# Optimization experiments

Measured on AMD Instinct MI355X. Metric: run time of the kernel, lower is better.

The kernel has to match this reference:

```python
import jax, jax.numpy as jnp
import numpy as np

B, N, D, C = 32, 6, 41, 64
FH, FW = 4, 6            # 150//32, 200//32
IN_CH = 768
NX, NY, NZ = 200, 200, 1 # from x/y/zbound
DX = np.array([0.5, 0.5, 20.0], np.float32)
BX = np.array([-49.75, -49.75, 0.0], np.float32)  # bound[0] + step/2


def _frustum():
    # (D, FH, FW, 3) pixel-coord + depth frustum, matching create_frustum
    ds = np.arange(4.0, 45.0, 1.0, dtype=np.float32)             # D = 41
    xs = np.linspace(0.0, 200.0 - 1.0, FW, dtype=np.float32)
    ys = np.linspace(0.0, 150.0 - 1.0, FH, dtype=np.float32)
    g = np.stack(np.broadcast_arrays(xs[None, None, :], ys[None, :, None], ds[:, None, None]), axis=-1)
    return jnp.asarray(g)


def setup_inputs() -> dict:
    key = jax.random.key(0)
    k1, k2, k3 = jax.random.split(key, 3)
    x = jax.random.normal(k1, (B, N, IN_CH, FH, FW), jnp.float32)
    # cam-to-ego base rotation (cam z -> ego x, cam x -> -ego y, cam y -> -ego z)
    R0 = np.array([[0., 0., 1.], [-1., 0., 0.], [0., -1., 0.]], np.float32)
    yaw = 2.0 * np.pi * np.arange(N) / N
    cz, sz = np.cos(yaw).astype(np.float32), np.sin(yaw).astype(np.float32)
    Rz = np.zeros((N, 3, 3), np.float32)
    Rz[:, 0, 0] = cz; Rz[:, 0, 1] = -sz; Rz[:, 1, 0] = sz; Rz[:, 1, 1] = cz; Rz[:, 2, 2] = 1.0
    rots = jnp.asarray(np.broadcast_to((Rz @ R0)[None], (B, N, 3, 3)))
    K = np.array([[100., 0., 100.], [0., 100., 75.], [0., 0., 1.]], np.float32)
    intrins = jnp.asarray(np.broadcast_to(K, (B, N, 3, 3)))
    trans = jax.random.uniform(k2, (B, N, 3), jnp.float32, -2.0, 2.0)
    conv_w = jax.random.normal(k3, (D + C, IN_CH), jnp.float32) * 0.02
    conv_b = jnp.zeros((D + C,), jnp.float32)
    return {"x": x, "rots": rots, "trans": trans, "intrins": intrins, "conv_w": conv_w, "conv_b": conv_b}


def reference(x, rots, trans, intrins, conv_w, conv_b):
    frustum = _frustum()                                        # (D,FH,FW,3)
    # --- get_geometry ---
    pts = jnp.concatenate([frustum[..., :2] * frustum[..., 2:3], frustum[..., 2:3]], -1)
    combine = rots @ jnp.linalg.inv(intrins)                    # (B,N,3,3)
    geom = jnp.einsum('bnij,dhwj->bndhwi', combine, pts) + trans[:, :, None, None, None, :]
    # --- get_cam_feats: 1x1 conv depthnet, softmax depth, outer product ---
    xf = x.reshape(B * N, IN_CH, FH, FW)
    y = jnp.einsum('oc,bchw->bohw', conv_w, xf) + conv_b[None, :, None, None]
    depth_logit = y[:, :D]                                      # (BN,D,FH,FW)
    depth = jax.nn.softmax(depth_logit, axis=1)
    feat = y[:, D:D + C]                                        # (BN,C,FH,FW)
    xv = (depth[:, None] * feat[:, :, None]).reshape(B, N, C, D, FH, FW).transpose(0, 1, 3, 4, 5, 2)
    # --- voxel_pooling: segment-sum over voxel rank, scatter to BEV ---
    xN = xv.reshape(-1, C)                                      # (Nprime, C)
    g = ((geom - (BX - DX / 2.0)) / DX).astype(jnp.int32).reshape(-1, 3)  # trunc like .long()
    Np = xN.shape[0]
    bix = jnp.repeat(jnp.arange(Np // (Np // B) * 0 + B), Np // B)        # batch index per point
    kept = ((g[:, 0] >= 0) & (g[:, 0] < NX) & (g[:, 1] >= 0) & (g[:, 1] < NY)
            & (g[:, 2] >= 0) & (g[:, 2] < NZ))
    idx = ((bix * NZ + g[:, 2]) * NX + g[:, 0]) * NY + g[:, 1]
    idx = jnp.where(kept, idx, 0)
    xm = jnp.where(kept[:, None], xN, 0.0)
    pooled = jax.ops.segment_sum(xm, idx, num_segments=B * NZ * NX * NY)  # (B*NZ*NX*NY, C)
    final = pooled.reshape(B, NZ, NX, NY, C).transpose(0, 1, 4, 2, 3).reshape(B, NZ * C, NX, NY)
    return (final, depth_logit)
```

## Files before the change

### kernel.cpp

```cpp
#include <hip/hip_runtime.h>
#include <hip/hip_bf16.h>

#define B_    32
#define N_    6
#define D_    41
#define C_    64
#define FH_   4
#define FW_   6
#define INCH  768
#define HW    24
#define O_    105
#define PBN   984
#define PPB   5904
#define NPTS  188928
#define FINAL_ELEMS 81920000
#define NSEG  8
#define SEGV  5000
#define CONVB 192


__global__ __launch_bounds__(256) void k_fused(
    const float* __restrict__ x, const float* __restrict__ w,
    const float* __restrict__ bias,
    const float* __restrict__ m1, const float* __restrict__ trans,
    const float* __restrict__ m2,
    float* __restrict__ feat_ws, float* __restrict__ depth_ws,
    float* __restrict__ dlogit,
    int* __restrict__ cnt, unsigned* __restrict__ entries)
{
    __shared__ float xs[9216];
    __shared__ float ys[O_ * HW];
    __shared__ float smax[HW], srs[HW];

    const int t = threadIdx.x;

    if (blockIdx.x < CONVB) {
        const int bn = blockIdx.x;
        const int og = t / 6;
        const int q6 = t % 6;

        float a[3][4] = {{0.f,0.f,0.f,0.f},{0.f,0.f,0.f,0.f},{0.f,0.f,0.f,0.f}};
        const int o0 = og * 3;
        const float4* wr0 = (const float4*)(w + (size_t)(o0 + 0) * INCH);
        const float4* wr1 = (const float4*)(w + (size_t)(o0 + 1) * INCH);
        const float4* wr2 = (const float4*)(w + (size_t)(o0 + 2) * INCH);
        float4* xs4 = (float4*)xs;

        for (int half = 0; half < 2; ++half) {
            if (half) __syncthreads();
            const float4* xg = (const float4*)(x + (size_t)bn * (INCH * HW)) + half * 2304;
            for (int i = t; i < 2304; i += 256) xs4[i] = xg[i];
            __syncthreads();

            if (t < 210) {
                const int wb = half * 96;
                for (int c4 = 0; c4 < 96; ++c4) {
                    float4 w0 = wr0[wb + c4];
                    float4 w1 = wr1[wb + c4];
                    float4 w2 = wr2[wb + c4];
                    int cb = c4 * 4;
                    float4 x0 = xs4[(cb + 0) * 6 + q6];
                    float4 x1 = xs4[(cb + 1) * 6 + q6];
                    float4 x2 = xs4[(cb + 2) * 6 + q6];
                    float4 x3 = xs4[(cb + 3) * 6 + q6];
                    a[0][0]=fmaf(w0.x,x0.x,a[0][0]); a[0][1]=fmaf(w0.x,x0.y,a[0][1]);
                    a[0][2]=fmaf(w0.x,x0.z,a[0][2]); a[0][3]=fmaf(w0.x,x0.w,a[0][3]);
                    a[1][0]=fmaf(w1.x,x0.x,a[1][0]); a[1][1]=fmaf(w1.x,x0.y,a[1][1]);
                    a[1][2]=fmaf(w1.x,x0.z,a[1][2]); a[1][3]=fmaf(w1.x,x0.w,a[1][3]);
                    a[2][0]=fmaf(w2.x,x0.x,a[2][0]); a[2][1]=fmaf(w2.x,x0.y,a[2][1]);
                    a[2][2]=fmaf(w2.x,x0.z,a[2][2]); a[2][3]=fmaf(w2.x,x0.w,a[2][3]);
                    a[0][0]=fmaf(w0.y,x1.x,a[0][0]); a[0][1]=fmaf(w0.y,x1.y,a[0][1]);
                    a[0][2]=fmaf(w0.y,x1.z,a[0][2]); a[0][3]=fmaf(w0.y,x1.w,a[0][3]);
                    a[1][0]=fmaf(w1.y,x1.x,a[1][0]); a[1][1]=fmaf(w1.y,x1.y,a[1][1]);
                    a[1][2]=fmaf(w1.y,x1.z,a[1][2]); a[1][3]=fmaf(w1.y,x1.w,a[1][3]);
                    a[2][0]=fmaf(w2.y,x1.x,a[2][0]); a[2][1]=fmaf(w2.y,x1.y,a[2][1]);
                    a[2][2]=fmaf(w2.y,x1.z,a[2][2]); a[2][3]=fmaf(w2.y,x1.w,a[2][3]);
                    a[0][0]=fmaf(w0.z,x2.x,a[0][0]); a[0][1]=fmaf(w0.z,x2.y,a[0][1]);
                    a[0][2]=fmaf(w0.z,x2.z,a[0][2]); a[0][3]=fmaf(w0.z,x2.w,a[0][3]);
                    a[1][0]=fmaf(w1.z,x2.x,a[1][0]); a[1][1]=fmaf(w1.z,x2.y,a[1][1]);
                    a[1][2]=fmaf(w1.z,x2.z,a[1][2]); a[1][3]=fmaf(w1.z,x2.w,a[1][3]);
                    a[2][0]=fmaf(w2.z,x2.x,a[2][0]); a[2][1]=fmaf(w2.z,x2.y,a[2][1]);
                    a[2][2]=fmaf(w2.z,x2.z,a[2][2]); a[2][3]=fmaf(w2.z,x2.w,a[2][3]);
                    a[0][0]=fmaf(w0.w,x3.x,a[0][0]); a[0][1]=fmaf(w0.w,x3.y,a[0][1]);
                    a[0][2]=fmaf(w0.w,x3.z,a[0][2]); a[0][3]=fmaf(w0.w,x3.w,a[0][3]);
                    a[1][0]=fmaf(w1.w,x3.x,a[1][0]); a[1][1]=fmaf(w1.w,x3.y,a[1][1]);
                    a[1][2]=fmaf(w1.w,x3.z,a[1][2]); a[1][3]=fmaf(w1.w,x3.w,a[1][3]);
                    a[2][0]=fmaf(w2.w,x3.x,a[2][0]); a[2][1]=fmaf(w2.w,x3.y,a[2][1]);
                    a[2][2]=fmaf(w2.w,x3.z,a[2][2]); a[2][3]=fmaf(w2.w,x3.w,a[2][3]);
                }
            }
        }

        if (t < 210) {
#pragma unroll
            for (int r = 0; r < 3; r++) {
                float bo = bias[o0 + r];
#pragma unroll
                for (int j = 0; j < 4; j++)
                    ys[(o0 + r) * HW + q6 * 4 + j] = a[r][j] + bo;
            }
        }
        __syncthreads();

        if (t < HW) {
            float mx = -1e30f;
            for (int d = 0; d < D_; d++) mx = fmaxf(mx, ys[d * HW + t]);
            float s = 0.f;
            for (int d = 0; d < D_; d++) s = __fadd_rn(s, expf(__fsub_rn(ys[d * HW + t], mx)));
            smax[t] = mx; srs[t] = s;
        }
        __syncthreads();

        for (int u = t; u < D_ * HW; u += 256) {
            float yv = ys[u];
            int hw = u % HW;
            depth_ws[bn * PBN + u] = __fdiv_rn(expf(__fsub_rn(yv, smax[hw])), srs[hw]);
            dlogit[(size_t)bn * PBN + u] = yv;
        }
        for (int u = t; u < C_ * HW; u += 256)
            feat_ws[(size_t)bn * (C_ * HW) + u] = ys[D_ * HW + u];
        return;
    }

    __shared__ int lcnt[16], lbase[16];

    const float* rots = (fabsf(m1[0]) > 50.0f) ? m2 : m1;
    const float* intr = (fabsf(m1[0]) > 50.0f) ? m1 : m2;

    const int gb0 = blockIdx.x - CONVB;
    int p = gb0 * 256 + t;
    if (t < 16) lcnt[t] = 0;
    __syncthreads();

    int b  = p / PPB;
    int pl = p % PPB;
    int n  = pl / PBN;
    int r  = pl % PBN;
    int d  = r / HW;
    int hw = r % HW;
    int h = hw / FW_, wp = hw % FW_;

    float dv = 4.0f + (float)d;
    float xi = (float)((double)wp * (199.0 / 5.0));
    float yi = (float)((double)h  * (149.0 / 3.0));
    float px = __fmul_rn(xi, dv), py = __fmul_rn(yi, dv), pz = dv;

    int bn = b * N_ + n;
    const float* K = intr + bn * 9;
    const float* R = rots + bn * 9;
    const float* T = trans + bn * 3;

    float a00 = K[0], a01 = K[1], a02 = K[2];
    float a11 = K[4], a12 = K[5];
    float a22 = K[8];

    float i00 = __fdiv_rn(1.0f, a00);
    float i11 = __fdiv_rn(1.0f, a11);
    float x0  = __fmul_rn(a01, i00);
    float i01 = __fmul_rn(-i11, x0);
    float i22 = __fdiv_rn(1.0f, a22);
    float y0  = __fmul_rn(a02, i00);
    y0 = __fadd_rn(y0, __fmul_rn(a12, i01));
    float y1  = __fmul_rn(a12, i11);
    float i02 = __fmul_rn(-i22, y0);
    float i12 = __fmul_rn(-i22, y1);
    float i10 = 0.f, i20 = 0.f, i21 = 0.f;

    float r00 = R[0], r01 = R[1], r02 = R[2];
    float r10 = R[3], r11 = R[4], r12 = R[5];
    float r20 = R[6], r21 = R[7], r22 = R[8];

#define MM(u0,u1,u2, v0,v1,v2) \
    __fmaf_rn(u2, v2, __fmaf_rn(u1, v1, __fmul_rn(u0, v0)))
    float c00 = MM(r00, r01, r02, i00, i10, i20);
    float c01 = MM(r00, r01, r02, i01, i11, i21);
    float c02 = MM(r00, r01, r02, i02, i12, i22);
    float c10 = MM(r10, r11, r12, i00, i10, i20);
    float c11 = MM(r10, r11, r12, i01, i11, i21);
    float c12 = MM(r10, r11, r12, i02, i12, i22);
    float c20 = MM(r20, r21, r22, i00, i10, i20);
    float c21 = MM(r20, r21, r22, i01, i11, i21);
    float c22 = MM(r20, r21, r22, i02, i12, i22);
#undef MM

#define DOT3(u0,v0,u1,v1,u2,v2) \
    __fadd_rn(__fadd_rn(__fmul_rn(u0,v0), __fmul_rn(u1,v1)), __fmul_rn(u2,v2))
    float gx = __fadd_rn(DOT3(c00,px, c01,py, c02,pz), T[0]);
    float gy = __fadd_rn(DOT3(c10,px, c11,py, c12,pz), T[1]);
    float gz = __fadd_rn(DOT3(c20,px, c21,py, c22,pz), T[2]);
#undef DOT3

    int ix = (int)__fmul_rn(__fadd_rn(gx, 50.0f), 2.0f);
    int iy = (int)__fmul_rn(__fadd_rn(gy, 50.0f), 2.0f);
    int iz = (int)__fdiv_rn(__fadd_rn(gz, 10.0f), 20.0f);
    bool kept = (ix >= 0) && (ix < 200) && (iy >= 0) && (iy < 200) && (iz == 0);

    const int bmin = (gb0 * 256) / PPB;
    int lb = 0, slot = 0;
    unsigned epack = 0;
    if (kept) {
        int vl  = ix * 200 + iy;
        int g   = vl / SEGV;
        int rel = vl - g * SEGV;
        int nhw = n * HW + hw;
        epack = (unsigned)rel | ((unsigned)nhw << 13) | ((unsigned)d << 21);
        lb  = (b - bmin) * NSEG + g;
        slot = atomicAdd(&lcnt[lb], 1);
    }
    __syncthreads();
    if (t < 16 && lcnt[t] > 0) {
        int gbk = (bmin + (t >> 3)) * NSEG + (t & 7);
        lbase[t] = atomicAdd(&cnt[gbk], lcnt[t]);
    }
    __syncthreads();
    if (kept) {
        int gbk = (bmin + (lb >> 3)) * NSEG + (lb & 7);
        entries[(size_t)gbk * PPB + lbase[lb] + slot] = epack;
    }
}

__global__ __launch_bounds__(256) void k_splat(
    const float* __restrict__ feat, const float* __restrict__ depth,
    const int* __restrict__ cnt, const unsigned* __restrict__ entries,
    float* __restrict__ out)
{
    __shared__ float plane[SEGV];
    __shared__ float ftab[144];
    int bid = blockIdx.x;
    int b   = bid >> 9;
    int rem = bid & 511;
    int c   = rem >> 3;
    int g   = rem & 7;
    int t   = threadIdx.x;
    float4* pl4 = (float4*)plane;

    for (int i = t; i < SEGV / 4; i += 256) pl4[i] = make_float4(0.f, 0.f, 0.f, 0.f);
    if (t < 144) {
        int n  = t / HW;
        int hw = t - n * HW;
        ftab[t] = feat[(size_t)(b * N_ + n) * (C_ * HW) + c * HW + hw];
    }
    __syncthreads();

    const int bkt = b * NSEG + g;
    const int ne = cnt[bkt];
    const unsigned* eb = entries + (size_t)bkt * PPB;
    const float* db = depth + (size_t)b * PPB;
    for (int i = t; i < ne; i += 256) {
        unsigned e = eb[i];
        int rel = e & 8191u;
        int nhw = (e >> 13) & 255u;
        int d   = e >> 21;
        int n   = nhw / HW;
        int hw  = nhw - n * HW;
        float dp = db[n * PBN + d * HW + hw];
        atomicAdd(&plane[rel], dp * ftab[nhw]);
    }
    __syncthreads();

    float4* ob = (float4*)(out + ((size_t)(b * C_ + c) * 40000) + g * SEGV);
    for (int i = t; i < SEGV / 4; i += 256) ob[i] = pl4[i];
}

extern "C" void kernel_launch(void* const* d_in, const int* in_sizes, int n_in,
                              void* d_out, int out_size, void* d_ws, size_t ws_size,
                              hipStream_t stream) {
    const float *x = nullptr, *m1 = nullptr, *m2 = nullptr, *trn = nullptr,
                *w = nullptr, *bias = nullptr;
    for (int i = 0; i < n_in; i++) {
        const float* p = (const float*)d_in[i];
        switch (in_sizes[i]) {
            case 3538944: x = p; break;
            case 1728:    if (!m1) m1 = p; else m2 = p; break;
            case 576:     trn = p; break;
            case 80640:   w = p; break;
            case 105:     bias = p; break;
            default: break;
        }
    }
    if (!x)    x    = (const float*)d_in[0];
    if (!m1)   m1   = (const float*)d_in[1];
    if (!trn)  trn  = (const float*)d_in[2];
    if (!m2)   m2   = (const float*)d_in[3];
    if (!w)    w    = (const float*)d_in[4];
    if (!bias) bias = (const float*)d_in[5];

    float*    feat_ws  = (float*)d_ws;
    float*    depth_ws = feat_ws + 192 * C_ * HW;
    int*      cnt      = (int*)(depth_ws + NPTS);
    unsigned* entries  = (unsigned*)(cnt + 256);

    float* out    = (float*)d_out;
    float* dlogit = out + FINAL_ELEMS;

    hipMemsetAsync(cnt, 0, 256 * sizeof(int), stream);
    k_fused<<<CONVB + 738, 256, 0, stream>>>(x, w, bias, m1, trn, m2,
                                             feat_ws, depth_ws, dlogit,
                                             cnt, entries);
    k_splat<<<16384, 256, 0, stream>>>(feat_ws, depth_ws, cnt, entries, out);
}
```

Before: 449.5 us.

## Split conv blocks by spatial row to quadruple conv parallelism

The depth/feature 1x1 conv now uses four blocks per camera image, one per feature-map row of six pixels, instead of one block per image. Each block transposes its six input columns into padded shared memory so every thread reads a contiguous channel vector, and it computes three outputs for one pixel across all 768 channels. The aim is to fill more compute units and shrink shared memory per block. In exchange each weight row is reloaded four times as often and each thread does less reuse per loaded weight.

Result: slower. 479.2 us (+6.6%).

```diff
diff --git a/kernel.cpp b/kernel.cpp
--- a/kernel.cpp
+++ b/kernel.cpp
@@ -16,7 +16,8 @@
 #define FINAL_ELEMS 81920000
 #define NSEG  8
 #define SEGV  5000
-#define CONVB 192
+#define CONVB 768
+#define XSL   772
 
 
 __global__ __launch_bounds__(256) void k_fused(
@@ -28,97 +29,72 @@
     float* __restrict__ dlogit,
     int* __restrict__ cnt, unsigned* __restrict__ entries)
 {
-    __shared__ float xs[9216];
-    __shared__ float ys[O_ * HW];
-    __shared__ float smax[HW], srs[HW];
+    __shared__ float xs[6 * XSL];
+    __shared__ float ys[O_ * 6];
+    __shared__ float smax[6], srs[6];
 
     const int t = threadIdx.x;
 
     if (blockIdx.x < CONVB) {
-        const int bn = blockIdx.x;
-        const int og = t / 6;
-        const int q6 = t % 6;
-
-        float a[3][4] = {{0.f,0.f,0.f,0.f},{0.f,0.f,0.f,0.f},{0.f,0.f,0.f,0.f}};
-        const int o0 = og * 3;
-        const float4* wr0 = (const float4*)(w + (size_t)(o0 + 0) * INCH);
-        const float4* wr1 = (const float4*)(w + (size_t)(o0 + 1) * INCH);
-        const float4* wr2 = (const float4*)(w + (size_t)(o0 + 2) * INCH);
-        float4* xs4 = (float4*)xs;
-
-        for (int half = 0; half < 2; ++half) {
-            if (half) __syncthreads();
-            const float4* xg = (const float4*)(x + (size_t)bn * (INCH * HW)) + half * 2304;
-            for (int i = t; i < 2304; i += 256) xs4[i] = xg[i];
-            __syncthreads();
-
-            if (t < 210) {
-                const int wb = half * 96;
-                for (int c4 = 0; c4 < 96; ++c4) {
-                    float4 w0 = wr0[wb + c4];
-                    float4 w1 = wr1[wb + c4];
-                    float4 w2 = wr2[wb + c4];
-                    int cb = c4 * 4;
-                    float4 x0 = xs4[(cb + 0) * 6 + q6];
-                    float4 x1 = xs4[(cb + 1) * 6 + q6];
-                    float4 x2 = xs4[(cb + 2) * 6 + q6];
-                    float4 x3 = xs4[(cb + 3) * 6 + q6];
-                    a[0][0]=fmaf(w0.x,x0.x,a[0][0]); a[0][1]=fmaf(w0.x,x0.y,a[0][1]);
-                    a[0][2]=fmaf(w0.x,x0.z,a[0][2]); a[0][3]=fmaf(w0.x,x0.w,a[0][3]);
-                    a[1][0]=fmaf(w1.x,x0.x,a[1][0]); a[1][1]=fmaf(w1.x,x0.y,a[1][1]);
-                    a[1][2]=fmaf(w1.x,x0.z,a[1][2]); a[1][3]=fmaf(w1.x,x0.w,a[1][3]);
-                    a[2][0]=fmaf(w2.x,x0.x,a[2][0]); a[2][1]=fmaf(w2.x,x0.y,a[2][1]);
-                    a[2][2]=fmaf(w2.x,x0.z,a[2][2]); a[2][3]=fmaf(w2.x,x0.w,a[2][3]);
-                    a[0][0]=fmaf(w0.y,x1.x,a[0][0]); a[0][1]=fmaf(w0.y,x1.y,a[0][1]);
-                    a[0][2]=fmaf(w0.y,x1.z,a[0][2]); a[0][3]=fmaf(w0.y,x1.w,a[0][3]);
-                    a[1][0]=fmaf(w1.y,x1.x,a[1][0]); a[1][1]=fmaf(w1.y,x1.y,a[1][1]);
-                    a[1][2]=fmaf(w1.y,x1.z,a[1][2]); a[1][3]=fmaf(w1.y,x1.w,a[1][3]);
-                    a[2][0]=fmaf(w2.y,x1.x,a[2][0]); a[2][1]=fmaf(w2.y,x1.y,a[2][1]);
-                    a[2][2]=fmaf(w2.y,x1.z,a[2][2]); a[2][3]=fmaf(w2.y,x1.w,a[2][3]);
-                    a[0][0]=fmaf(w0.z,x2.x,a[0][0]); a[0][1]=fmaf(w0.z,x2.y,a[0][1]);
-                    a[0][2]=fmaf(w0.z,x2.z,a[0][2]); a[0][3]=fmaf(w0.z,x2.w,a[0][3]);
-                    a[1][0]=fmaf(w1.z,x2.x,a[1][0]); a[1][1]=fmaf(w1.z,x2.y,a[1][1]);
-                    a[1][2]=fmaf(w1.z,x2.z,a[1][2]); a[1][3]=fmaf(w1.z,x2.w,a[1][3]);
-                    a[2][0]=fmaf(w2.z,x2.x,a[2][0]); a[2][1]=fmaf(w2.z,x2.y,a[2][1]);
-                    a[2][2]=fmaf(w2.z,x2.z,a[2][2]); a[2][3]=fmaf(w2.z,x2.w,a[2][3]);
-                    a[0][0]=fmaf(w0.w,x3.x,a[0][0]); a[0][1]=fmaf(w0.w,x3.y,a[0][1]);
-                    a[0][2]=fmaf(w0.w,x3.z,a[0][2]); a[0][3]=fmaf(w0.w,x3.w,a[0][3]);
-                    a[1][0]=fmaf(w1.w,x3.x,a[1][0]); a[1][1]=fmaf(w1.w,x3.y,a[1][1]);
-                    a[1][2]=fmaf(w1.w,x3.z,a[1][2]); a[1][3]=fmaf(w1.w,x3.w,a[1][3]);
-                    a[2][0]=fmaf(w2.w,x3.x,a[2][0]); a[2][1]=fmaf(w2.w,x3.y,a[2][1]);
-                    a[2][2]=fmaf(w2.w,x3.z,a[2][2]); a[2][3]=fmaf(w2.w,x3.w,a[2][3]);
-                }
+        const int bn = blockIdx.x >> 2;
+        const int q  = blockIdx.x & 3;
+        const int og  = t / 6;
+        const int col = t % 6;
+
+        const float2* xg2 = (const float2*)(x + (size_t)bn * (INCH * HW));
+        for (int i = t; i < 2304; i += 256) {
+            int c = i / 3, j = i - c * 3;
+            float2 v = xg2[c * 12 + q * 3 + j];
+            xs[(2 * j + 0) * XSL + c] = v.x;
+            xs[(2 * j + 1) * XSL + c] = v.y;
+        }
+        __syncthreads();
+
+        if (t < 210) {
+            const int o0 = og * 3;
+            const float4* wr0 = (const float4*)(w + (size_t)(o0 + 0) * INCH);
+            const float4* wr1 = (const float4*)(w + (size_t)(o0 + 1) * INCH);
+            const float4* wr2 = (const float4*)(w + (size_t)(o0 + 2) * INCH);
+            const float* xcol = xs + col * XSL;
+            float a0 = 0.f, a1 = 0.f, a2 = 0.f;
+            for (int c4 = 0; c4 < 192; ++c4) {
+                float4 w0 = wr0[c4];
+                float4 w1 = wr1[c4];
+                float4 w2 = wr2[c4];
+                float4 xv = *(const float4*)(xcol + c4 * 4);
+                a0 = fmaf(w0.x, xv.x, a0); a0 = fmaf(w0.y, xv.y, a0);
+                a0 = fmaf(w0.z, xv.z, a0); a0 = fmaf(w0.w, xv.w, a0);
+                a1 = fmaf(w1.x, xv.x, a1); a1 = fmaf(w1.y, xv.y, a1);
+                a1 = fmaf(w1.z, xv.z, a1); a1 = fmaf(w1.w, xv.w, a1);
+                a2 = fmaf(w2.x, xv.x, a2); a2 = fmaf(w2.y, xv.y, a2);
+                a2 = fmaf(w2.z, xv.z, a2); a2 = fmaf(w2.w, xv.w, a2);
             }
-        }
-
-        if (t < 210) {
-#pragma unroll
-            for (int r = 0; r < 3; r++) {
-                float bo = bias[o0 + r];
-#pragma unroll
-                for (int j = 0; j < 4; j++)
-                    ys[(o0 + r) * HW + q6 * 4 + j] = a[r][j] + bo;
-            }
+            ys[(o0 + 0) * 6 + col] = a0 + bias[o0 + 0];
+            ys[(o0 + 1) * 6 + col] = a1 + bias[o0 + 1];
+            ys[(o0 + 2) * 6 + col] = a2 + bias[o0 + 2];
         }
         __syncthreads();
 
-        if (t < HW) {
+        if (t < 6) {
             float mx = -1e30f;
-            for (int d = 0; d < D_; d++) mx = fmaxf(mx, ys[d * HW + t]);
+            for (int d = 0; d < D_; d++) mx = fmaxf(mx, ys[d * 6 + t]);
             float s = 0.f;
-            for (int d = 0; d < D_; d++) s = __fadd_rn(s, expf(__fsub_rn(ys[d * HW + t], mx)));
+            for (int d = 0; d < D_; d++) s = __fadd_rn(s, expf(__fsub_rn(ys[d * 6 + t], mx)));
             smax[t] = mx; srs[t] = s;
         }
         __syncthreads();
 
-        for (int u = t; u < D_ * HW; u += 256) {
+        for (int u = t; u < D_ * 6; u += 256) {
+            int d = u / 6, col2 = u - d * 6;
             float yv = ys[u];
-            int hw = u % HW;
-            depth_ws[bn * PBN + u] = __fdiv_rn(expf(__fsub_rn(yv, smax[hw])), srs[hw]);
-            dlogit[(size_t)bn * PBN + u] = yv;
-        }
-        for (int u = t; u < C_ * HW; u += 256)
-            feat_ws[(size_t)bn * (C_ * HW) + u] = ys[D_ * HW + u];
+            int gidx = bn * PBN + d * HW + q * 6 + col2;
+            depth_ws[gidx] = __fdiv_rn(expf(__fsub_rn(yv, smax[col2])), srs[col2]);
+            dlogit[(size_t)gidx] = yv;
+        }
+        for (int u = t; u < C_ * 6; u += 256) {
+            int c = u / 6, col2 = u - c * 6;
+            feat_ws[(size_t)bn * (C_ * HW) + c * HW + q * 6 + col2] = ys[(D_ + c) * 6 + col2];
+        }
         return;
     }
 
```

## Bucket voxels into 240-cell chunks and splat all channels per block

Applied to the files above, without the earlier changes.

The splat stage no longer launches one block per (batch, channel, 5000-voxel segment), each rescanning the same entry list. It now launches one block per (batch, 240-voxel chunk) that holds all 64 channels in a padded shared-memory tile. Features are stored channel-innermost so each entry is read once and the 64 channels are accumulated by neighbouring threads. This removes 64-fold redundant entry and depth reads, at the cost of strided output writes during the transpose-out and more bucket atomics in the geometry blocks. Entry buckets are capped at 2048 slots, which risks overflow if too many points land in one chunk.

New measurement: 469.4 us. 1.04x slower.

```diff
diff --git a/kernel.cpp b/kernel.cpp
--- a/kernel.cpp
+++ b/kernel.cpp
@@ -14,9 +14,12 @@
 #define PPB   5904
 #define NPTS  188928
 #define FINAL_ELEMS 81920000
-#define NSEG  8
-#define SEGV  5000
 #define CONVB 192
+#define CH    240
+#define NCH   167
+#define NBKT  (B_ * NCH)
+#define ESTR  2048
+#define PLS   65
 
 
 __global__ __launch_bounds__(256) void k_fused(
@@ -31,6 +34,7 @@
     __shared__ float xs[9216];
     __shared__ float ys[O_ * HW];
     __shared__ float smax[HW], srs[HW];
+    __shared__ int lcnt[2 * NCH], lbase[2 * NCH];
 
     const int t = threadIdx.x;
 
@@ -117,19 +121,20 @@
             depth_ws[bn * PBN + u] = __fdiv_rn(expf(__fsub_rn(yv, smax[hw])), srs[hw]);
             dlogit[(size_t)bn * PBN + u] = yv;
         }
-        for (int u = t; u < C_ * HW; u += 256)
-            feat_ws[(size_t)bn * (C_ * HW) + u] = ys[D_ * HW + u];
+        for (int u = t; u < C_ * HW; u += 256) {
+            int hw = u >> 6;
+            int c  = u & 63;
+            feat_ws[(size_t)(bn * HW + hw) * C_ + c] = ys[(D_ + c) * HW + hw];
+        }
         return;
     }
-
-    __shared__ int lcnt[16], lbase[16];
 
     const float* rots = (fabsf(m1[0]) > 50.0f) ? m2 : m1;
     const float* intr = (fabsf(m1[0]) > 50.0f) ? m1 : m2;
 
     const int gb0 = blockIdx.x - CONVB;
     int p = gb0 * 256 + t;
-    if (t < 16) lcnt[t] = 0;
+    for (int i = t; i < 2 * NCH; i += 256) lcnt[i] = 0;
     __syncthreads();
 
     int b  = p / PPB;
@@ -200,22 +205,20 @@
     unsigned epack = 0;
     if (kept) {
         int vl  = ix * 200 + iy;
-        int g   = vl / SEGV;
-        int rel = vl - g * SEGV;
-        int nhw = n * HW + hw;
-        epack = (unsigned)rel | ((unsigned)nhw << 13) | ((unsigned)d << 21);
-        lb  = (b - bmin) * NSEG + g;
+        int g   = vl / CH;
+        int rel = vl - g * CH;
+        epack = (unsigned)rel | ((unsigned)n << 8) | ((unsigned)hw << 11)
+              | ((unsigned)d << 16);
+        lb  = (b - bmin) * NCH + g;
         slot = atomicAdd(&lcnt[lb], 1);
     }
     __syncthreads();
-    if (t < 16 && lcnt[t] > 0) {
-        int gbk = (bmin + (t >> 3)) * NSEG + (t & 7);
-        lbase[t] = atomicAdd(&cnt[gbk], lcnt[t]);
-    }
+    for (int i = t; i < 2 * NCH; i += 256)
+        if (lcnt[i] > 0)
+            lbase[i] = atomicAdd(&cnt[bmin * NCH + i], lcnt[i]);
     __syncthreads();
     if (kept) {
-        int gbk = (bmin + (lb >> 3)) * NSEG + (lb & 7);
-        entries[(size_t)gbk * PPB + lbase[lb] + slot] = epack;
+        entries[(size_t)(bmin * NCH + lb) * ESTR + lbase[lb] + slot] = epack;
     }
 }
 
@@ -224,42 +227,41 @@
     const int* __restrict__ cnt, const unsigned* __restrict__ entries,
     float* __restrict__ out)
 {
-    __shared__ float plane[SEGV];
-    __shared__ float ftab[144];
-    int bid = blockIdx.x;
-    int b   = bid >> 9;
-    int rem = bid & 511;
-    int c   = rem >> 3;
-    int g   = rem & 7;
-    int t   = threadIdx.x;
+    __shared__ float plane[CH * PLS];
+    const int bid = blockIdx.x;
+    const int b   = bid / NCH;
+    const int g   = bid - b * NCH;
+    const int t   = threadIdx.x;
     float4* pl4 = (float4*)plane;
 
-    for (int i = t; i < SEGV / 4; i += 256) pl4[i] = make_float4(0.f, 0.f, 0.f, 0.f);
-    if (t < 144) {
-        int n  = t / HW;
-        int hw = t - n * HW;
-        ftab[t] = feat[(size_t)(b * N_ + n) * (C_ * HW) + c * HW + hw];
-    }
-    __syncthreads();
-
-    const int bkt = b * NSEG + g;
+    for (int i = t; i < (CH * PLS) / 4; i += 256)
+        pl4[i] = make_float4(0.f, 0.f, 0.f, 0.f);
+    __syncthreads();
+
+    const int bkt = b * NCH + g;
     const int ne = cnt[bkt];
-    const unsigned* eb = entries + (size_t)bkt * PPB;
+    const unsigned* eb = entries + (size_t)bkt * ESTR;
     const float* db = depth + (size_t)b * PPB;
-    for (int i = t; i < ne; i += 256) {
+    const float* fb = feat + (size_t)b * (N_ * HW * C_);
+    const int c = t & 63;
+    for (int i = (t >> 6); i < ne; i += 4) {
         unsigned e = eb[i];
-        int rel = e & 8191u;
-        int nhw = (e >> 13) & 255u;
-        int d   = e >> 21;
-        int n   = nhw / HW;
-        int hw  = nhw - n * HW;
+        int rel = e & 255u;
+        int n   = (e >> 8) & 7u;
+        int hw  = (e >> 11) & 31u;
+        int d   = (e >> 16) & 63u;
         float dp = db[n * PBN + d * HW + hw];
-        atomicAdd(&plane[rel], dp * ftab[nhw]);
-    }
-    __syncthreads();
-
-    float4* ob = (float4*)(out + ((size_t)(b * C_ + c) * 40000) + g * SEGV);
-    for (int i = t; i < SEGV / 4; i += 256) ob[i] = pl4[i];
+        float fv = fb[(n * HW + hw) * C_ + c];
+        atomicAdd(&plane[rel * PLS + c], dp * fv);
+    }
+    __syncthreads();
+
+    const int base = g * CH;
+    for (int i = t; i < C_ * CH; i += 256) {
+        int cc = i / CH, v = i - cc * CH;
+        if (base + v < 40000)
+            out[((size_t)(b * C_ + cc)) * 40000 + base + v] = plane[v * PLS + cc];
+    }
 }
 
 extern "C" void kernel_launch(void* const* d_in, const int* in_sizes, int n_in,
@@ -288,14 +290,14 @@
     float*    feat_ws  = (float*)d_ws;
     float*    depth_ws = feat_ws + 192 * C_ * HW;
     int*      cnt      = (int*)(depth_ws + NPTS);
-    unsigned* entries  = (unsigned*)(cnt + 256);
+    unsigned* entries  = (unsigned*)(cnt + NBKT);
 
     float* out    = (float*)d_out;
     float* dlogit = out + FINAL_ELEMS;
 
-    hipMemsetAsync(cnt, 0, 256 * sizeof(int), stream);
+    hipMemsetAsync(cnt, 0, NBKT * sizeof(int), stream);
     k_fused<<<CONVB + 738, 256, 0, stream>>>(x, w, bias, m1, trn, m2,
                                              feat_ws, depth_ws, dlogit,
                                              cnt, entries);
-    k_splat<<<16384, 256, 0, stream>>>(feat_ws, depth_ws, cnt, entries, out);
+    k_splat<<<NBKT, 256, 0, stream>>>(feat_ws, depth_ws, cnt, entries, out);
 }
```
